# Kernel tuning notes

Measured on AMD Instinct MI355X. Metric: run time of the kernel, lower is better.

The kernel has to match this reference:

```python
import jax, jax.numpy as jnp
import numpy as np

N_NODES = 100000
N_EDGES = 1600000
D = 128
L = 2


def setup_inputs() -> dict:
    key = jax.random.key(0)
    ks = jax.random.split(key, 8)
    s = 1.0 / np.sqrt(D)
    return {
        "x": jax.random.normal(ks[0], (N_NODES, D), dtype=jnp.float32),
        "edge_index": jax.random.randint(ks[1], (2, N_EDGES), 0, N_NODES, dtype=jnp.int64),
        "edge_weight": jax.random.uniform(ks[2], (N_EDGES,), dtype=jnp.float32),
        "weight": jax.random.normal(ks[3], (L, D, D), dtype=jnp.float32) * s,
        "w_ih": jax.random.normal(ks[4], (3 * D, D), dtype=jnp.float32) * s,
        "w_hh": jax.random.normal(ks[5], (3 * D, D), dtype=jnp.float32) * s,
        "b_ih": jax.random.normal(ks[6], (3 * D,), dtype=jnp.float32) * s,
        "b_hh": jax.random.normal(ks[7], (3 * D,), dtype=jnp.float32) * s,
    }


def _gru_cell(m, h, w_ih, w_hh, b_ih, b_hh):
    # torch.nn.GRUCell: gates ordered (reset, update, new)
    gi = m @ w_ih.T + b_ih  # [N, 3D]
    gh = h @ w_hh.T + b_hh  # [N, 3D]
    i_r, i_z, i_n = jnp.split(gi, 3, axis=-1)
    h_r, h_z, h_n = jnp.split(gh, 3, axis=-1)
    r = jax.nn.sigmoid(i_r + h_r)
    z = jax.nn.sigmoid(i_z + h_z)
    n = jnp.tanh(i_n + r * h_n)
    return (1.0 - z) * n + z * h


def reference(x, edge_index, edge_weight, weight, w_ih, w_hh, b_ih, b_hh):
    src = edge_index[0]
    dst = edge_index[1]
    h = x  # in_channels == out_channels, no zero-padding needed
    for i in range(L):
        m = h @ weight[i]                          # [N, D]
        msg = m[src] * edge_weight[:, None]        # [E, D] gather + scale
        agg = jax.ops.segment_sum(msg, dst, num_segments=N_NODES)  # scatter-add
        h = _gru_cell(agg, h, w_ih, w_hh, b_ih, b_hh)
    return h
```

## Files before the change

kernel.cpp:

```cpp
#include <hip/hip_runtime.h>
#include <hip/hip_bf16.h>
#include <stdint.h>

typedef unsigned short u16;
typedef unsigned long long u64;
typedef __attribute__((ext_vector_type(8))) short bf16x8;
typedef __attribute__((ext_vector_type(4))) float f32x4;

#define DD 128
#define NB 256
#define SB 10240

__device__ __forceinline__ u16 f2bf(float f){
  uint32_t u = __float_as_uint(f);
  uint32_t r = (u + 0x7fffu + ((u >> 16) & 1u)) >> 16;
  return (u16)r;
}
__device__ __forceinline__ float bf2f(u16 h){ return __uint_as_float(((uint32_t)h) << 16); }

struct Frag2 { bf16x8 hi, lo; };

__device__ __forceinline__ Frag2 split8(float4 v0, float4 v1){
  union { float f[8]; uint32_t u[8]; } U;
  *(float4*)&U.f[0] = v0; *(float4*)&U.f[4] = v1;
  union { uint32_t w[4]; bf16x8 v; } H, L;
  #pragma unroll
  for (int q = 0; q < 4; q++){
    uint32_t a = U.u[2*q], b = U.u[2*q+1];
    H.w[q] = __builtin_amdgcn_perm(b, a, 0x07060302);
    float l0 = U.f[2*q]   - __uint_as_float(a & 0xffff0000u);
    float l1 = U.f[2*q+1] - __uint_as_float(b & 0xffff0000u);
    L.w[q] = __builtin_amdgcn_perm(__float_as_uint(l1), __float_as_uint(l0), 0x07060302);
  }
  Frag2 r; r.hi = H.v; r.lo = L.v; return r;
}

__device__ __forceinline__ Frag2 load_afrag_g(const float* A, int row, int k0){
  const float4* p = (const float4*)(A + (size_t)row * DD + k0);
  return split8(p[0], p[1]);
}

__global__ void pack_kernel(const float* __restrict__ w, const float* __restrict__ wih,
                            const float* __restrict__ whh, const float* __restrict__ bih,
                            const float* __restrict__ bhh, u16* __restrict__ wtb,
                            u16* __restrict__ ihb, u16* __restrict__ hhb,
                            float* __restrict__ bias, int* __restrict__ gcursor, int L){
  int tid = blockIdx.x * 256 + threadIdx.x;
  int lane = tid & 63;
  int b1 = L * 2048, b2 = b1 + 6144, b3 = b2 + 6144, b4 = b3 + 512, b5 = b4 + NB;
  if (tid < b1){
    int kc = (tid >> 6) & 3, t = (tid >> 8) & 7, l = tid >> 11;
    int col = t*16 + (lane & 15), kb = kc*32 + 8*(lane >> 4);
    #pragma unroll
    for (int e = 0; e < 8; e++)
      wtb[(size_t)tid*8 + e] = f2bf(w[(size_t)l*DD*DD + (size_t)(kb + e)*DD + col]);
  } else if (tid < b2){
    int id = tid - b1;
    int kc = (id >> 6) & 3, t = id >> 8;
    int row = t*16 + (lane & 15), kb = kc*32 + 8*(lane >> 4);
    #pragma unroll
    for (int e = 0; e < 8; e++)
      ihb[(size_t)id*8 + e] = f2bf(wih[(size_t)row*DD + kb + e]);
  } else if (tid < b3){
    int id = tid - b2;
    int kc = (id >> 6) & 3, t = id >> 8;
    int row = t*16 + (lane & 15), kb = kc*32 + 8*(lane >> 4);
    #pragma unroll
    for (int e = 0; e < 8; e++)
      hhb[(size_t)id*8 + e] = f2bf(whh[(size_t)row*DD + kb + e]);
  } else if (tid < b4){
    int id = tid - b3;
    if (id < 256)      bias[id] = bih[id] + bhh[id];
    else if (id < 384) bias[id] = bih[id];
    else               bias[id] = bhh[id - 128];
  } else if (tid < b5){
    gcursor[tid - b4] = 0;
  }
}

__global__ __launch_bounds__(256) void binA_kernel(const int* __restrict__ src,
    const int* __restrict__ dst, const float* __restrict__ ew,
    int* __restrict__ gcursor, u64* __restrict__ staging, int E, int N){
  __shared__ unsigned lcnt[NB];
  __shared__ unsigned lbase[NB];
  __shared__ unsigned lcur[NB];
  __shared__ unsigned gbase[NB];
  __shared__ unsigned char sbucket[4096];
  __shared__ u64 sedge[4096];
  const int CH = 4096;
  int tid = threadIdx.x;
  int e0 = blockIdx.x * CH;

  lcnt[tid] = 0;
  __syncthreads();
  for (int i = tid; i < CH; i += 256){
    int e = e0 + i;
    if (e < E){
      unsigned d = (unsigned)dst[e];
      if (d < (unsigned)N) atomicAdd(&lcnt[d >> 9], 1u);
    }
  }
  __syncthreads();
  lbase[tid] = lcnt[tid];
  __syncthreads();
  for (int off = 1; off < NB; off <<= 1){
    unsigned t = (tid >= off) ? lbase[tid - off] : 0u;
    __syncthreads();
    lbase[tid] += t;
    __syncthreads();
  }
  unsigned total = lbase[NB - 1];
  lbase[tid] -= lcnt[tid];
  gbase[tid] = (unsigned)atomicAdd(&gcursor[tid], (int)lcnt[tid]);
  lcur[tid] = lbase[tid];
  __syncthreads();
  for (int i = tid; i < CH; i += 256){
    int e = e0 + i;
    if (e < E){
      unsigned d = (unsigned)dst[e];
      if (d < (unsigned)N){
        unsigned b = d >> 9;
        unsigned p = atomicAdd(&lcur[b], 1u);
        unsigned s = (unsigned)src[e];
        sedge[p] = ((u64)__float_as_uint(ew[e]) << 32) | ((u64)(s & 0x1FFFFu) << 9)
                 | (u64)(d & 0x1FFu);
        sbucket[p] = (unsigned char)b;
      }
    }
  }
  __syncthreads();
  for (int i = tid; i < (int)total; i += 256){
    unsigned b = sbucket[i];
    unsigned gpos = gbase[b] + ((unsigned)i - lbase[b]);
    if (gpos < SB) staging[(size_t)b*SB + gpos] = sedge[i];
  }
}

__global__ __launch_bounds__(256) void binB_kernel(const u64* __restrict__ staging,
    const int* __restrict__ gcursor, int* __restrict__ row_ptr,
    uint2* __restrict__ entries, int N, int E){
  __shared__ int sg[NB];
  __shared__ unsigned ncnt[512];
  __shared__ unsigned nsc[512];
  __shared__ unsigned ncur[512];
  int tid = threadIdx.x;
  int b = blockIdx.x;
  sg[tid] = gcursor[tid];
  __syncthreads();
  for (int off = 1; off < NB; off <<= 1){
    int t = (tid >= off) ? sg[tid - off] : 0;
    __syncthreads();
    sg[tid] += t;
    __syncthreads();
  }
  int cnt = gcursor[b];
  if (cnt > SB) cnt = SB;
  int base = sg[b] - cnt;
  if (b == NB - 1 && tid == 0) row_ptr[N] = sg[NB - 1];
  const u64* st = staging + (size_t)b * SB;

  ncnt[tid] = 0; ncnt[tid + 256] = 0;
  __syncthreads();
  for (int i = tid; i < cnt; i += 256)
    atomicAdd(&ncnt[(unsigned)(st[i] & 0x1FFu)], 1u);
  __syncthreads();
  nsc[tid] = ncnt[tid]; nsc[tid + 256] = ncnt[tid + 256];
  __syncthreads();
  for (int off = 1; off < 512; off <<= 1){
    unsigned t0 = (tid >= off) ? nsc[tid - off] : 0u;
    unsigned t1 = (tid + 256 >= off) ? nsc[tid + 256 - off] : 0u;
    __syncthreads();
    nsc[tid] += t0; nsc[tid + 256] += t1;
    __syncthreads();
  }
  #pragma unroll
  for (int h = 0; h < 2; h++){
    int k = tid + h*256;
    unsigned excl = nsc[k] - ncnt[k];
    int g = b*512 + k;
    if (g < N) row_ptr[g] = base + (int)excl;
    ncur[k] = excl;
  }
  __syncthreads();
  for (int i = tid; i < cnt; i += 256){
    u64 v = st[i];
    unsigned local = (unsigned)(v & 0x1FFu);
    unsigned p = atomicAdd(&ncur[local], 1u);
    uint2 ent;
    ent.x = (unsigned)((v >> 9) & 0x1FFFFu);
    ent.y = (unsigned)(v >> 32);
    entries[base + p] = ent;
  }
}

__global__ __launch_bounds__(256) void gemm_m_kernel(const float* __restrict__ hin,
    const u16* __restrict__ wb, u16* __restrict__ mout, int nstripes){
  __shared__ u16 lw[32*512];
  int lane = threadIdx.x & 63;
  int wid = threadIdx.x >> 6;
  int stripe = blockIdx.x*4 + wid;
  bool active = stripe < nstripes;
  int n0 = (active ? stripe : (nstripes - 1)) * 16;
  int lrow = lane & 15, lk = lane >> 4;

  bf16x8 sreg[8];
  #pragma unroll
  for (int b = 0; b < 8; b++){
    int q = wid*8 + b;
    sreg[b] = *(const bf16x8*)(wb + ((size_t)q*64 + lane)*8);
  }
  Frag2 a[4];
  #pragma unroll
  for (int kc = 0; kc < 4; kc++)
    a[kc] = load_afrag_g(hin, n0 + lrow, kc*32 + 8*lk);
  #pragma unroll
  for (int b = 0; b < 8; b++){
    int q = wid*8 + b;
    *(bf16x8*)(lw + ((size_t)q*64 + lane)*8) = sreg[b];
  }
  __syncthreads();

  f32x4 zero = {0.f, 0.f, 0.f, 0.f};
  f32x4 acc[8];
  #pragma unroll
  for (int t = 0; t < 8; t++) acc[t] = zero;
  #pragma unroll
  for (int kc = 0; kc < 4; kc++){
    #pragma unroll
    for (int t = 0; t < 8; t++){
      bf16x8 b = *(const bf16x8*)(lw + ((size_t)(t*4 + kc)*64 + lane)*8);
      acc[t] = __builtin_amdgcn_mfma_f32_16x16x32_bf16(a[kc].hi, b, acc[t], 0, 0, 0);
      acc[t] = __builtin_amdgcn_mfma_f32_16x16x32_bf16(a[kc].lo, b, acc[t], 0, 0, 0);
    }
  }
  if (active){
    #pragma unroll
    for (int t = 0; t < 8; t++){
      #pragma unroll
      for (int r = 0; r < 4; r++)
        mout[(size_t)(n0 + lk*4 + r)*DD + t*16 + lrow] = f2bf(acc[t][r]);
    }
  }
}

__global__ __launch_bounds__(256) void gather_kernel(const int* __restrict__ row_ptr,
    const uint2* __restrict__ entries, const u16* __restrict__ mbf,
    float* __restrict__ agg, int N){
  int lane = threadIdx.x & 63;
  int node = (blockIdx.x*256 + threadIdx.x) >> 6;
  if (node >= N) return;
  int s = row_ptr[node], e = row_ptr[node + 1];
  float al[8], ah[8];
  #pragma unroll
  for (int u = 0; u < 8; u++){ al[u] = 0.f; ah[u] = 0.f; }
  int i = s;
  for (; i + 16 <= e; i += 16){
    uint2 en[16];
    #pragma unroll
    for (int u = 0; u < 16; u++) en[u] = entries[i + u];
    uint32_t mv[16];
    #pragma unroll
    for (int u = 0; u < 16; u++)
      mv[u] = *(const uint32_t*)(mbf + (size_t)en[u].x*DD + 2*lane);
    #pragma unroll
    for (int u = 0; u < 16; u++){
      float wv = __uint_as_float(en[u].y);
      al[u & 7] += wv * bf2f((u16)(mv[u] & 0xffffu));
      ah[u & 7] += wv * bf2f((u16)(mv[u] >> 16));
    }
  }
  for (; i + 8 <= e; i += 8){
    uint2 en[8];
    #pragma unroll
    for (int u = 0; u < 8; u++) en[u] = entries[i + u];
    uint32_t mv[8];
    #pragma unroll
    for (int u = 0; u < 8; u++)
      mv[u] = *(const uint32_t*)(mbf + (size_t)en[u].x*DD + 2*lane);
    #pragma unroll
    for (int u = 0; u < 8; u++){
      float wv = __uint_as_float(en[u].y);
      al[u] += wv * bf2f((u16)(mv[u] & 0xffffu));
      ah[u] += wv * bf2f((u16)(mv[u] >> 16));
    }
  }
  for (; i < e; i++){
    uint2 ent = entries[i];
    float wv = __uint_as_float(ent.y);
    uint32_t mv = *(const uint32_t*)(mbf + (size_t)ent.x*DD + 2*lane);
    al[0] += wv * bf2f((u16)(mv & 0xffffu));
    ah[0] += wv * bf2f((u16)(mv >> 16));
  }
  float2 o;
  o.x = ((al[0]+al[1]) + (al[2]+al[3])) + ((al[4]+al[5]) + (al[6]+al[7]));
  o.y = ((ah[0]+ah[1]) + (ah[2]+ah[3])) + ((ah[4]+ah[5]) + (ah[6]+ah[7]));
  *(float2*)(agg + (size_t)node*DD + 2*lane) = o;
}

__global__ __launch_bounds__(256, 4) void gru_kernel(
    const float* __restrict__ agg, const float* hin,
    const u16* __restrict__ ihb, const u16* __restrict__ hhb,
    const float* __restrict__ bias, float* hout, int nstripes){
  __shared__ u16 lw[2][12*512];
  int lane = threadIdx.x & 63;
  int wid = threadIdx.x >> 6;
  int stripe = blockIdx.x*4 + wid;
  bool active = stripe < nstripes;
  int n0 = (active ? stripe : (nstripes - 1)) * 16;
  int lrow = lane & 15, lk = lane >> 4;

  Frag2 aa[4], ahf[4];
  #pragma unroll
  for (int kc = 0; kc < 4; kc++){
    int k0 = kc*32 + 8*lk;
    aa[kc]  = load_afrag_g(agg, n0 + lrow, k0);
    ahf[kc] = load_afrag_g(hin, n0 + lrow, k0);
  }

  int q = wid*3;
  int g0 = q >> 2,       kc0 = q & 3;
  int g1 = (q+1) >> 2,   kc1 = (q+1) & 3;
  int g2 = (q+2) >> 2,   kc2 = (q+2) & 3;

  {
    bf16x8 s0 = *(const bf16x8*)(ihb + ((size_t)((g0*8 + 0)*4 + kc0)*64 + lane)*8);
    bf16x8 s1 = *(const bf16x8*)(ihb + ((size_t)((g1*8 + 0)*4 + kc1)*64 + lane)*8);
    bf16x8 s2 = *(const bf16x8*)(ihb + ((size_t)((g2*8 + 0)*4 + kc2)*64 + lane)*8);
    *(bf16x8*)(lw[0] + ((size_t)(q+0)*64 + lane)*8) = s0;
    *(bf16x8*)(lw[0] + ((size_t)(q+1)*64 + lane)*8) = s1;
    *(bf16x8*)(lw[0] + ((size_t)(q+2)*64 + lane)*8) = s2;
  }
  __syncthreads();

  f32x4 zero = {0.f, 0.f, 0.f, 0.f};
  f32x4 ir = zero, iz = zero, in_ = zero, hr = zero, hz = zero, hn = zero;
  for (int ph = 0; ph < 16; ph++){
    int jt = ph >> 1, half = ph & 1;
    bf16x8 n0r, n1r, n2r;
    if (ph < 15){
      int njt = (ph + 1) >> 1;
      const u16* wsrc = ((ph + 1) & 1) ? hhb : ihb;
      n0r = *(const bf16x8*)(wsrc + ((size_t)((g0*8 + njt)*4 + kc0)*64 + lane)*8);
      n1r = *(const bf16x8*)(wsrc + ((size_t)((g1*8 + njt)*4 + kc1)*64 + lane)*8);
      n2r = *(const bf16x8*)(wsrc + ((size_t)((g2*8 + njt)*4 + kc2)*64 + lane)*8);
    }
    const u16* buf = lw[ph & 1];
    if (half == 0){
      ir = zero; iz = zero; in_ = zero;
      #pragma unroll
      for (int kc = 0; kc < 4; kc++){
        bf16x8 b0 = *(const bf16x8*)(buf + ((size_t)(0*4 + kc)*64 + lane)*8);
        bf16x8 b1 = *(const bf16x8*)(buf + ((size_t)(1*4 + kc)*64 + lane)*8);
        bf16x8 b2 = *(const bf16x8*)(buf + ((size_t)(2*4 + kc)*64 + lane)*8);
        ir  = __builtin_amdgcn_mfma_f32_16x16x32_bf16(aa[kc].hi, b0, ir,  0, 0, 0);
        ir  = __builtin_amdgcn_mfma_f32_16x16x32_bf16(aa[kc].lo, b0, ir,  0, 0, 0);
        iz  = __builtin_amdgcn_mfma_f32_16x16x32_bf16(aa[kc].hi, b1, iz,  0, 0, 0);
        iz  = __builtin_amdgcn_mfma_f32_16x16x32_bf16(aa[kc].lo, b1, iz,  0, 0, 0);
        in_ = __builtin_amdgcn_mfma_f32_16x16x32_bf16(aa[kc].hi, b2, in_, 0, 0, 0);
        in_ = __builtin_amdgcn_mfma_f32_16x16x32_bf16(aa[kc].lo, b2, in_, 0, 0, 0);
      }
    } else {
      hr = zero; hz = zero; hn = zero;
      #pragma unroll
      for (int kc = 0; kc < 4; kc++){
        bf16x8 b0 = *(const bf16x8*)(buf + ((size_t)(0*4 + kc)*64 + lane)*8);
        bf16x8 b1 = *(const bf16x8*)(buf + ((size_t)(1*4 + kc)*64 + lane)*8);
        bf16x8 b2 = *(const bf16x8*)(buf + ((size_t)(2*4 + kc)*64 + lane)*8);
        hr = __builtin_amdgcn_mfma_f32_16x16x32_bf16(ahf[kc].hi, b0, hr, 0, 0, 0);
        hr = __builtin_amdgcn_mfma_f32_16x16x32_bf16(ahf[kc].lo, b0, hr, 0, 0, 0);
        hz = __builtin_amdgcn_mfma_f32_16x16x32_bf16(ahf[kc].hi, b1, hz, 0, 0, 0);
        hz = __builtin_amdgcn_mfma_f32_16x16x32_bf16(ahf[kc].lo, b1, hz, 0, 0, 0);
        hn = __builtin_amdgcn_mfma_f32_16x16x32_bf16(ahf[kc].hi, b2, hn, 0, 0, 0);
        hn = __builtin_amdgcn_mfma_f32_16x16x32_bf16(ahf[kc].lo, b2, hn, 0, 0, 0);
      }
      if (active){
        int j = jt*16 + lrow;
        float br = bias[j];
        float bz = bias[128 + j];
        float bi = bias[256 + j];
        float bh = bias[384 + j];
        #pragma unroll
        for (int r = 0; r < 4; r++){
          int node = n0 + lk*4 + r;
          float xr = ir[r] + hr[r] + br;
          float xz = iz[r] + hz[r] + bz;
          float rg = __builtin_amdgcn_rcpf(1.f + __expf(-xr));
          float zg = __builtin_amdgcn_rcpf(1.f + __expf(-xz));
          float xn = in_[r] + bi + rg*(hn[r] + bh);
          xn = fminf(fmaxf(xn, -30.f), 30.f);
          float e2 = __expf(2.f*xn);
          float ng = 1.f - 2.f*__builtin_amdgcn_rcpf(e2 + 1.f);
          float hv = hin[(size_t)node*DD + j];
          hout[(size_t)node*DD + j] = ng + zg*(hv - ng);
        }
      }
    }
    if (ph < 15){
      u16* nbuf = lw[(ph + 1) & 1];
      *(bf16x8*)(nbuf + ((size_t)(q+0)*64 + lane)*8) = n0r;
      *(bf16x8*)(nbuf + ((size_t)(q+1)*64 + lane)*8) = n1r;
      *(bf16x8*)(nbuf + ((size_t)(q+2)*64 + lane)*8) = n2r;
    }
    __syncthreads();
  }
}

extern "C" void kernel_launch(void* const* d_in, const int* in_sizes, int n_in,
                              void* d_out, int out_size, void* d_ws, size_t ws_size,
                              hipStream_t stream){
  const float* x   = (const float*)d_in[0];
  const int*   ei  = (const int*)d_in[1];
  const float* ew  = (const float*)d_in[2];
  const float* wgt = (const float*)d_in[3];
  const float* wih = (const float*)d_in[4];
  const float* whh = (const float*)d_in[5];
  const float* bih = (const float*)d_in[6];
  const float* bhh = (const float*)d_in[7];
  float* out = (float*)d_out;

  const int N = in_sizes[0] / DD;
  const int E = in_sizes[2];
  const int L = in_sizes[3] / (DD * DD);

  char* p = (char*)d_ws;
  auto alloc = [&](size_t b) -> char* {
    char* r = p; p += (b + 255) & ~(size_t)255; return r;
  };
  u16*   wtb     = (u16*)  alloc((size_t)L * 2048 * 8 * 2);
  u16*   ihb     = (u16*)  alloc((size_t)6144 * 8 * 2);
  u16*   hhb     = (u16*)  alloc((size_t)6144 * 8 * 2);
  float* bias    = (float*)alloc(512 * 4);
  int*   gcursor = (int*)  alloc(NB * 4);
  int*   row_ptr = (int*)  alloc(((size_t)N + 1) * 4);
  uint2* entries = (uint2*)alloc((size_t)E * 8);
  u16*   mbf     = (u16*)  alloc((size_t)N * DD * 2);
  float* agg     = (float*)alloc((size_t)N * DD * 4);
  u64*   staging = (u64*)agg;

  const int* src = ei;
  const int* dst = ei + E;

  int packN = L*2048 + 6144 + 6144 + 512 + NB;
  pack_kernel<<<(packN + 255)/256, 256, 0, stream>>>(wgt, wih, whh, bih, bhh,
                                                     wtb, ihb, hhb, bias, gcursor, L);
  binA_kernel<<<(E + 4095)/4096, 256, 0, stream>>>(src, dst, ew, gcursor, staging, E, N);
  binB_kernel<<<NB, 256, 0, stream>>>(staging, gcursor, row_ptr, entries, N, E);

  int nstripes = N / 16;
  int ggrid = (nstripes + 3) / 4;
  for (int l = 0; l < L; l++){
    const float* hin = (l == 0) ? x : out;
    gemm_m_kernel<<<ggrid, 256, 0, stream>>>(hin, wtb + (size_t)l*2048*8, mbf, nstripes);
    gather_kernel<<<(N*64 + 255)/256, 256, 0, stream>>>(row_ptr, entries, mbf, agg, N);
    gru_kernel<<<ggrid, 256, 0, stream>>>(agg, hin, ihb, hhb, bias, out, nstripes);
  }
}
```

Baseline: 380.3 us.

## Slice node features into column strips and pack edge entries into 32-bit words

```diff
diff --git a/kernel.cpp b/kernel.cpp
--- a/kernel.cpp
+++ b/kernel.cpp
@@ -138,7 +138,7 @@
 
 __global__ __launch_bounds__(256) void binB_kernel(const u64* __restrict__ staging,
     const int* __restrict__ gcursor, int* __restrict__ row_ptr,
-    uint2* __restrict__ entries, int N, int E){
+    uint32_t* __restrict__ entries, int N, int E){
   __shared__ int sg[NB];
   __shared__ unsigned ncnt[512];
   __shared__ unsigned nsc[512];
@@ -186,15 +186,16 @@
     u64 v = st[i];
     unsigned local = (unsigned)(v & 0x1FFu);
     unsigned p = atomicAdd(&ncur[local], 1u);
-    uint2 ent;
-    ent.x = (unsigned)((v >> 9) & 0x1FFFFu);
-    ent.y = (unsigned)(v >> 32);
-    entries[base + p] = ent;
+    unsigned s = (unsigned)((v >> 9) & 0x1FFFFu);
+    float w = __uint_as_float((unsigned)(v >> 32));
+    unsigned wq = (unsigned)(w * 32768.f + 0.5f);
+    if (wq > 32767u) wq = 32767u;
+    entries[base + p] = (s << 15) | wq;
   }
 }
 
 __global__ __launch_bounds__(256) void gemm_m_kernel(const float* __restrict__ hin,
-    const u16* __restrict__ wb, u16* __restrict__ mout, int nstripes){
+    const u16* __restrict__ wb, u16* __restrict__ msb, int nstripes, int N){
   __shared__ u16 lw[32*512];
   int lane = threadIdx.x & 63;
   int wid = threadIdx.x >> 6;
@@ -238,63 +239,58 @@
     for (int t = 0; t < 8; t++){
       #pragma unroll
       for (int r = 0; r < 4; r++)
-        mout[(size_t)(n0 + lk*4 + r)*DD + t*16 + lrow] = f2bf(acc[t][r]);
-    }
-  }
-}
-
-__global__ __launch_bounds__(256) void gather_kernel(const int* __restrict__ row_ptr,
-    const uint2* __restrict__ entries, const u16* __restrict__ mbf,
+        msb[(size_t)t*N*16 + (size_t)(n0 + lk*4 + r)*16 + lrow] = f2bf(acc[t][r]);
+    }
+  }
+}
+
+__global__ __launch_bounds__(512) void gather_kernel(const int* __restrict__ row_ptr,
+    const uint32_t* __restrict__ entries, const u16* __restrict__ msb,
     float* __restrict__ agg, int N){
   int lane = threadIdx.x & 63;
-  int node = (blockIdx.x*256 + threadIdx.x) >> 6;
-  if (node >= N) return;
-  int s = row_ptr[node], e = row_ptr[node + 1];
-  float al[8], ah[8];
-  #pragma unroll
-  for (int u = 0; u < 8; u++){ al[u] = 0.f; ah[u] = 0.f; }
-  int i = s;
-  for (; i + 16 <= e; i += 16){
-    uint2 en[16];
-    #pragma unroll
-    for (int u = 0; u < 16; u++) en[u] = entries[i + u];
-    uint32_t mv[16];
-    #pragma unroll
-    for (int u = 0; u < 16; u++)
-      mv[u] = *(const uint32_t*)(mbf + (size_t)en[u].x*DD + 2*lane);
-    #pragma unroll
-    for (int u = 0; u < 16; u++){
-      float wv = __uint_as_float(en[u].y);
-      al[u & 7] += wv * bf2f((u16)(mv[u] & 0xffffu));
-      ah[u & 7] += wv * bf2f((u16)(mv[u] >> 16));
-    }
-  }
-  for (; i + 8 <= e; i += 8){
-    uint2 en[8];
-    #pragma unroll
-    for (int u = 0; u < 8; u++) en[u] = entries[i + u];
-    uint32_t mv[8];
-    #pragma unroll
-    for (int u = 0; u < 8; u++)
-      mv[u] = *(const uint32_t*)(mbf + (size_t)en[u].x*DD + 2*lane);
-    #pragma unroll
-    for (int u = 0; u < 8; u++){
-      float wv = __uint_as_float(en[u].y);
-      al[u] += wv * bf2f((u16)(mv[u] & 0xffffu));
-      ah[u] += wv * bf2f((u16)(mv[u] >> 16));
-    }
-  }
-  for (; i < e; i++){
-    uint2 ent = entries[i];
-    float wv = __uint_as_float(ent.y);
-    uint32_t mv = *(const uint32_t*)(mbf + (size_t)ent.x*DD + 2*lane);
-    al[0] += wv * bf2f((u16)(mv & 0xffffu));
-    ah[0] += wv * bf2f((u16)(mv >> 16));
-  }
-  float2 o;
-  o.x = ((al[0]+al[1]) + (al[2]+al[3])) + ((al[4]+al[5]) + (al[6]+al[7]));
-  o.y = ((ah[0]+ah[1]) + (ah[2]+ah[3])) + ((ah[4]+ah[5]) + (ah[6]+ah[7]));
-  *(float2*)(agg + (size_t)node*DD + 2*lane) = o;
+  int wid = threadIdx.x >> 6;
+  int s = blockIdx.x & 7;
+  int slot = (blockIdx.x >> 3)*8 + wid;
+  const u16* ms = msb + (size_t)s*N*16;
+  int g = lane >> 3;
+  int c = lane & 7;
+
+  for (int node = slot; node < N; node += 8192){
+    int s0 = row_ptr[node], e0 = row_ptr[node + 1];
+    float a0 = 0.f, a1 = 0.f;
+    int i = s0;
+    for (; i + 16 <= e0; i += 16){
+      unsigned w0 = entries[i + g];
+      unsigned w1 = entries[i + 8 + g];
+      uint32_t m0 = *(const uint32_t*)(ms + (size_t)(w0 >> 15)*16 + 2*c);
+      uint32_t m1 = *(const uint32_t*)(ms + (size_t)(w1 >> 15)*16 + 2*c);
+      float f0 = (float)(w0 & 0x7fffu) * (1.f/32768.f);
+      float f1 = (float)(w1 & 0x7fffu) * (1.f/32768.f);
+      a0 += f0 * __uint_as_float(m0 << 16);
+      a1 += f0 * __uint_as_float(m0 & 0xffff0000u);
+      a0 += f1 * __uint_as_float(m1 << 16);
+      a1 += f1 * __uint_as_float(m1 & 0xffff0000u);
+    }
+    for (; i < e0; i += 8){
+      int idx = i + g;
+      if (idx < e0){
+        unsigned w0 = entries[idx];
+        uint32_t m0 = *(const uint32_t*)(ms + (size_t)(w0 >> 15)*16 + 2*c);
+        float f0 = (float)(w0 & 0x7fffu) * (1.f/32768.f);
+        a0 += f0 * __uint_as_float(m0 << 16);
+        a1 += f0 * __uint_as_float(m0 & 0xffff0000u);
+      }
+    }
+    #pragma unroll
+    for (int msk = 8; msk < 64; msk <<= 1){
+      a0 += __shfl_xor(a0, msk);
+      a1 += __shfl_xor(a1, msk);
+    }
+    if (lane < 8){
+      float2 o; o.x = a0; o.y = a1;
+      *(float2*)(agg + (size_t)node*DD + s*16 + 2*c) = o;
+    }
+  }
 }
 
 __global__ __launch_bounds__(256, 4) void gru_kernel(
@@ -426,16 +422,16 @@
   auto alloc = [&](size_t b) -> char* {
     char* r = p; p += (b + 255) & ~(size_t)255; return r;
   };
-  u16*   wtb     = (u16*)  alloc((size_t)L * 2048 * 8 * 2);
-  u16*   ihb     = (u16*)  alloc((size_t)6144 * 8 * 2);
-  u16*   hhb     = (u16*)  alloc((size_t)6144 * 8 * 2);
-  float* bias    = (float*)alloc(512 * 4);
-  int*   gcursor = (int*)  alloc(NB * 4);
-  int*   row_ptr = (int*)  alloc(((size_t)N + 1) * 4);
-  uint2* entries = (uint2*)alloc((size_t)E * 8);
-  u16*   mbf     = (u16*)  alloc((size_t)N * DD * 2);
-  float* agg     = (float*)alloc((size_t)N * DD * 4);
-  u64*   staging = (u64*)agg;
+  u16*      wtb     = (u16*)     alloc((size_t)L * 2048 * 8 * 2);
+  u16*      ihb     = (u16*)     alloc((size_t)6144 * 8 * 2);
+  u16*      hhb     = (u16*)     alloc((size_t)6144 * 8 * 2);
+  float*    bias    = (float*)   alloc(512 * 4);
+  int*      gcursor = (int*)     alloc(NB * 4);
+  int*      row_ptr = (int*)     alloc(((size_t)N + 1) * 4);
+  uint32_t* entries = (uint32_t*)alloc((size_t)E * 4);
+  u16*      msb     = (u16*)     alloc((size_t)N * DD * 2);
+  float*    agg     = (float*)   alloc((size_t)N * DD * 4);
+  u64*      staging = (u64*)agg;
 
   const int* src = ei;
   const int* dst = ei + E;
@@ -450,8 +446,8 @@
   int ggrid = (nstripes + 3) / 4;
   for (int l = 0; l < L; l++){
     const float* hin = (l == 0) ? x : out;
-    gemm_m_kernel<<<ggrid, 256, 0, stream>>>(hin, wtb + (size_t)l*2048*8, mbf, nstripes);
-    gather_kernel<<<(N*64 + 255)/256, 256, 0, stream>>>(row_ptr, entries, mbf, agg, N);
+    gemm_m_kernel<<<ggrid, 256, 0, stream>>>(hin, wtb + (size_t)l*2048*8, msb, nstripes, N);
+    gather_kernel<<<8192, 512, 0, stream>>>(row_ptr, entries, msb, agg, N);
     gru_kernel<<<ggrid, 256, 0, stream>>>(agg, hin, ihb, hhb, bias, out, nstripes);
   }
 }
```

After: 560.2 us. 1.47x slower.

## Triple-buffer GRU weight tiles and fully unroll the gate loop

Applied to the files above, without the earlier changes.

```diff
diff --git a/kernel.cpp b/kernel.cpp
--- a/kernel.cpp
+++ b/kernel.cpp
@@ -301,7 +301,7 @@
     const float* __restrict__ agg, const float* hin,
     const u16* __restrict__ ihb, const u16* __restrict__ hhb,
     const float* __restrict__ bias, float* hout, int nstripes){
-  __shared__ u16 lw[2][12*512];
+  __shared__ u16 lw[3][12*512];
   int lane = threadIdx.x & 63;
   int wid = threadIdx.x >> 6;
   int stripe = blockIdx.x*4 + wid;
@@ -321,85 +321,104 @@
   int g0 = q >> 2,       kc0 = q & 3;
   int g1 = (q+1) >> 2,   kc1 = (q+1) & 3;
   int g2 = (q+2) >> 2,   kc2 = (q+2) & 3;
-
+  size_t lo0 = ((size_t)(q+0)*64 + lane)*8;
+  size_t lo1 = ((size_t)(q+1)*64 + lane)*8;
+  size_t lo2 = ((size_t)(q+2)*64 + lane)*8;
+
+  bf16x8 rH0, rH1, rH2;
   {
-    bf16x8 s0 = *(const bf16x8*)(ihb + ((size_t)((g0*8 + 0)*4 + kc0)*64 + lane)*8);
-    bf16x8 s1 = *(const bf16x8*)(ihb + ((size_t)((g1*8 + 0)*4 + kc1)*64 + lane)*8);
-    bf16x8 s2 = *(const bf16x8*)(ihb + ((size_t)((g2*8 + 0)*4 + kc2)*64 + lane)*8);
-    *(bf16x8*)(lw[0] + ((size_t)(q+0)*64 + lane)*8) = s0;
-    *(bf16x8*)(lw[0] + ((size_t)(q+1)*64 + lane)*8) = s1;
-    *(bf16x8*)(lw[0] + ((size_t)(q+2)*64 + lane)*8) = s2;
+    bf16x8 i0 = *(const bf16x8*)(ihb + ((size_t)((g0*8 + 0)*4 + kc0)*64 + lane)*8);
+    bf16x8 i1 = *(const bf16x8*)(ihb + ((size_t)((g1*8 + 0)*4 + kc1)*64 + lane)*8);
+    bf16x8 i2 = *(const bf16x8*)(ihb + ((size_t)((g2*8 + 0)*4 + kc2)*64 + lane)*8);
+    rH0 = *(const bf16x8*)(hhb + ((size_t)((g0*8 + 0)*4 + kc0)*64 + lane)*8);
+    rH1 = *(const bf16x8*)(hhb + ((size_t)((g1*8 + 0)*4 + kc1)*64 + lane)*8);
+    rH2 = *(const bf16x8*)(hhb + ((size_t)((g2*8 + 0)*4 + kc2)*64 + lane)*8);
+    *(bf16x8*)(lw[0] + lo0) = i0;
+    *(bf16x8*)(lw[0] + lo1) = i1;
+    *(bf16x8*)(lw[0] + lo2) = i2;
+    *(bf16x8*)(lw[1] + lo0) = rH0;
+    *(bf16x8*)(lw[1] + lo1) = rH1;
+    *(bf16x8*)(lw[1] + lo2) = rH2;
   }
   __syncthreads();
 
   f32x4 zero = {0.f, 0.f, 0.f, 0.f};
-  f32x4 ir = zero, iz = zero, in_ = zero, hr = zero, hz = zero, hn = zero;
-  for (int ph = 0; ph < 16; ph++){
-    int jt = ph >> 1, half = ph & 1;
-    bf16x8 n0r, n1r, n2r;
-    if (ph < 15){
-      int njt = (ph + 1) >> 1;
-      const u16* wsrc = ((ph + 1) & 1) ? hhb : ihb;
-      n0r = *(const bf16x8*)(wsrc + ((size_t)((g0*8 + njt)*4 + kc0)*64 + lane)*8);
-      n1r = *(const bf16x8*)(wsrc + ((size_t)((g1*8 + njt)*4 + kc1)*64 + lane)*8);
-      n2r = *(const bf16x8*)(wsrc + ((size_t)((g2*8 + njt)*4 + kc2)*64 + lane)*8);
-    }
-    const u16* buf = lw[ph & 1];
-    if (half == 0){
-      ir = zero; iz = zero; in_ = zero;
+  f32x4 ir = zero, iz = zero, in_ = zero;
+  #pragma unroll
+  for (int j = 0; j < 8; j++){
+    const u16* bufE = lw[(2*j) % 3];
+    u16* bufO = lw[(2*j + 1) % 3];
+    u16* bufE2 = lw[(2*j + 2) % 3];
+
+    bf16x8 nI0, nI1, nI2, nH0, nH1, nH2;
+    if (j < 7){
+      int njt = j + 1;
+      nI0 = *(const bf16x8*)(ihb + ((size_t)((g0*8 + njt)*4 + kc0)*64 + lane)*8);
+      nI1 = *(const bf16x8*)(ihb + ((size_t)((g1*8 + njt)*4 + kc1)*64 + lane)*8);
+      nI2 = *(const bf16x8*)(ihb + ((size_t)((g2*8 + njt)*4 + kc2)*64 + lane)*8);
+      nH0 = *(const bf16x8*)(hhb + ((size_t)((g0*8 + njt)*4 + kc0)*64 + lane)*8);
+      nH1 = *(const bf16x8*)(hhb + ((size_t)((g1*8 + njt)*4 + kc1)*64 + lane)*8);
+      nH2 = *(const bf16x8*)(hhb + ((size_t)((g2*8 + njt)*4 + kc2)*64 + lane)*8);
+    }
+    ir = zero; iz = zero; in_ = zero;
+    #pragma unroll
+    for (int kc = 0; kc < 4; kc++){
+      bf16x8 b0 = *(const bf16x8*)(bufE + ((size_t)(0*4 + kc)*64 + lane)*8);
+      bf16x8 b1 = *(const bf16x8*)(bufE + ((size_t)(1*4 + kc)*64 + lane)*8);
+      bf16x8 b2 = *(const bf16x8*)(bufE + ((size_t)(2*4 + kc)*64 + lane)*8);
+      ir  = __builtin_amdgcn_mfma_f32_16x16x32_bf16(aa[kc].hi, b0, ir,  0, 0, 0);
+      ir  = __builtin_amdgcn_mfma_f32_16x16x32_bf16(aa[kc].lo, b0, ir,  0, 0, 0);
+      iz  = __builtin_amdgcn_mfma_f32_16x16x32_bf16(aa[kc].hi, b1, iz,  0, 0, 0);
+      iz  = __builtin_amdgcn_mfma_f32_16x16x32_bf16(aa[kc].lo, b1, iz,  0, 0, 0);
+      in_ = __builtin_amdgcn_mfma_f32_16x16x32_bf16(aa[kc].hi, b2, in_, 0, 0, 0);
+      in_ = __builtin_amdgcn_mfma_f32_16x16x32_bf16(aa[kc].lo, b2, in_, 0, 0, 0);
+    }
+    if (j > 0){
+      *(bf16x8*)(bufO + lo0) = rH0;
+      *(bf16x8*)(bufO + lo1) = rH1;
+      *(bf16x8*)(bufO + lo2) = rH2;
+    }
+    __syncthreads();
+
+    f32x4 hr = zero, hz = zero, hn = zero;
+    #pragma unroll
+    for (int kc = 0; kc < 4; kc++){
+      bf16x8 b0 = *(const bf16x8*)(bufO + ((size_t)(0*4 + kc)*64 + lane)*8);
+      bf16x8 b1 = *(const bf16x8*)(bufO + ((size_t)(1*4 + kc)*64 + lane)*8);
+      bf16x8 b2 = *(const bf16x8*)(bufO + ((size_t)(2*4 + kc)*64 + lane)*8);
+      hr = __builtin_amdgcn_mfma_f32_16x16x32_bf16(ahf[kc].hi, b0, hr, 0, 0, 0);
+      hr = __builtin_amdgcn_mfma_f32_16x16x32_bf16(ahf[kc].lo, b0, hr, 0, 0, 0);
+      hz = __builtin_amdgcn_mfma_f32_16x16x32_bf16(ahf[kc].hi, b1, hz, 0, 0, 0);
+      hz = __builtin_amdgcn_mfma_f32_16x16x32_bf16(ahf[kc].lo, b1, hz, 0, 0, 0);
+      hn = __builtin_amdgcn_mfma_f32_16x16x32_bf16(ahf[kc].hi, b2, hn, 0, 0, 0);
+      hn = __builtin_amdgcn_mfma_f32_16x16x32_bf16(ahf[kc].lo, b2, hn, 0, 0, 0);
+    }
+    if (active){
+      int jj = j*16 + lrow;
+      float br = bias[jj];
+      float bz = bias[128 + jj];
+      float bi = bias[256 + jj];
+      float bh = bias[384 + jj];
       #pragma unroll
-      for (int kc = 0; kc < 4; kc++){
-        bf16x8 b0 = *(const bf16x8*)(buf + ((size_t)(0*4 + kc)*64 + lane)*8);
-        bf16x8 b1 = *(const bf16x8*)(buf + ((size_t)(1*4 + kc)*64 + lane)*8);
-        bf16x8 b2 = *(const bf16x8*)(buf + ((size_t)(2*4 + kc)*64 + lane)*8);
-        ir  = __builtin_amdgcn_mfma_f32_16x16x32_bf16(aa[kc].hi, b0, ir,  0, 0, 0);
-        ir  = __builtin_amdgcn_mfma_f32_16x16x32_bf16(aa[kc].lo, b0, ir,  0, 0, 0);
-        iz  = __builtin_amdgcn_mfma_f32_16x16x32_bf16(aa[kc].hi, b1, iz,  0, 0, 0);
-        iz  = __builtin_amdgcn_mfma_f32_16x16x32_bf16(aa[kc].lo, b1, iz,  0, 0, 0);
-        in_ = __builtin_amdgcn_mfma_f32_16x16x32_bf16(aa[kc].hi, b2, in_, 0, 0, 0);
-        in_ = __builtin_amdgcn_mfma_f32_16x16x32_bf16(aa[kc].lo, b2, in_, 0, 0, 0);
+      for (int r = 0; r < 4; r++){
+        int node = n0 + lk*4 + r;
+        float xr = ir[r] + hr[r] + br;
+        float xz = iz[r] + hz[r] + bz;
+        float rg = __builtin_amdgcn_rcpf(1.f + __expf(-xr));
+        float zg = __builtin_amdgcn_rcpf(1.f + __expf(-xz));
+        float xn = in_[r] + bi + rg*(hn[r] + bh);
+        xn = fminf(fmaxf(xn, -30.f), 30.f);
+        float e2 = __expf(2.f*xn);
+        float ng = 1.f - 2.f*__builtin_amdgcn_rcpf(e2 + 1.f);
+        float hv = hin[(size_t)node*DD + jj];
+        hout[(size_t)node*DD + jj] = ng + zg*(hv - ng);
       }
-    } else {
-      hr = zero; hz = zero; hn = zero;
-      #pragma unroll
-      for (int kc = 0; kc < 4; kc++){
-        bf16x8 b0 = *(const bf16x8*)(buf + ((size_t)(0*4 + kc)*64 + lane)*8);
-        bf16x8 b1 = *(const bf16x8*)(buf + ((size_t)(1*4 + kc)*64 + lane)*8);
-        bf16x8 b2 = *(const bf16x8*)(buf + ((size_t)(2*4 + kc)*64 + lane)*8);
-        hr = __builtin_amdgcn_mfma_f32_16x16x32_bf16(ahf[kc].hi, b0, hr, 0, 0, 0);
-        hr = __builtin_amdgcn_mfma_f32_16x16x32_bf16(ahf[kc].lo, b0, hr, 0, 0, 0);
-        hz = __builtin_amdgcn_mfma_f32_16x16x32_bf16(ahf[kc].hi, b1, hz, 0, 0, 0);
-        hz = __builtin_amdgcn_mfma_f32_16x16x32_bf16(ahf[kc].lo, b1, hz, 0, 0, 0);
-        hn = __builtin_amdgcn_mfma_f32_16x16x32_bf16(ahf[kc].hi, b2, hn, 0, 0, 0);
-        hn = __builtin_amdgcn_mfma_f32_16x16x32_bf16(ahf[kc].lo, b2, hn, 0, 0, 0);
-      }
-      if (active){
-        int j = jt*16 + lrow;
-        float br = bias[j];
-        float bz = bias[128 + j];
-        float bi = bias[256 + j];
-        float bh = bias[384 + j];
-        #pragma unroll
-        for (int r = 0; r < 4; r++){
-          int node = n0 + lk*4 + r;
-          float xr = ir[r] + hr[r] + br;
-          float xz = iz[r] + hz[r] + bz;
-          float rg = __builtin_amdgcn_rcpf(1.f + __expf(-xr));
-          float zg = __builtin_amdgcn_rcpf(1.f + __expf(-xz));
-          float xn = in_[r] + bi + rg*(hn[r] + bh);
-          xn = fminf(fmaxf(xn, -30.f), 30.f);
-          float e2 = __expf(2.f*xn);
-          float ng = 1.f - 2.f*__builtin_amdgcn_rcpf(e2 + 1.f);
-          float hv = hin[(size_t)node*DD + j];
-          hout[(size_t)node*DD + j] = ng + zg*(hv - ng);
-        }
-      }
-    }
-    if (ph < 15){
-      u16* nbuf = lw[(ph + 1) & 1];
-      *(bf16x8*)(nbuf + ((size_t)(q+0)*64 + lane)*8) = n0r;
-      *(bf16x8*)(nbuf + ((size_t)(q+1)*64 + lane)*8) = n1r;
-      *(bf16x8*)(nbuf + ((size_t)(q+2)*64 + lane)*8) = n2r;
+    }
+    if (j < 7){
+      *(bf16x8*)(bufE2 + lo0) = nI0;
+      *(bf16x8*)(bufE2 + lo1) = nI1;
+      *(bf16x8*)(bufE2 + lo2) = nI2;
+      rH0 = nH0; rH1 = nH1; rH2 = nH2;
     }
     __syncthreads();
   }
```

Result: slower. 405.9 us (+6.7%).

## Gather four edges per wavefront with 16-byte row loads and shuffle-reduce

Applied to the files above, without the earlier changes.

```diff
diff --git a/kernel.cpp b/kernel.cpp
--- a/kernel.cpp
+++ b/kernel.cpp
@@ -235,9 +235,9 @@
   }
   if (active){
     #pragma unroll
-    for (int t = 0; t < 8; t++){
+    for (int r = 0; r < 4; r++){
       #pragma unroll
-      for (int r = 0; r < 4; r++)
+      for (int t = 0; t < 8; t++)
         mout[(size_t)(n0 + lk*4 + r)*DD + t*16 + lrow] = f2bf(acc[t][r]);
     }
   }
@@ -247,54 +247,41 @@
     const uint2* __restrict__ entries, const u16* __restrict__ mbf,
     float* __restrict__ agg, int N){
   int lane = threadIdx.x & 63;
+  int q = lane >> 4;
+  int t = lane & 15;
   int node = (blockIdx.x*256 + threadIdx.x) >> 6;
   if (node >= N) return;
   int s = row_ptr[node], e = row_ptr[node + 1];
-  float al[8], ah[8];
-  #pragma unroll
-  for (int u = 0; u < 8; u++){ al[u] = 0.f; ah[u] = 0.f; }
-  int i = s;
-  for (; i + 16 <= e; i += 16){
-    uint2 en[16];
-    #pragma unroll
-    for (int u = 0; u < 16; u++) en[u] = entries[i + u];
-    uint32_t mv[16];
-    #pragma unroll
-    for (int u = 0; u < 16; u++)
-      mv[u] = *(const uint32_t*)(mbf + (size_t)en[u].x*DD + 2*lane);
-    #pragma unroll
-    for (int u = 0; u < 16; u++){
-      float wv = __uint_as_float(en[u].y);
-      al[u & 7] += wv * bf2f((u16)(mv[u] & 0xffffu));
-      ah[u & 7] += wv * bf2f((u16)(mv[u] >> 16));
-    }
-  }
-  for (; i + 8 <= e; i += 8){
-    uint2 en[8];
-    #pragma unroll
-    for (int u = 0; u < 8; u++) en[u] = entries[i + u];
-    uint32_t mv[8];
-    #pragma unroll
-    for (int u = 0; u < 8; u++)
-      mv[u] = *(const uint32_t*)(mbf + (size_t)en[u].x*DD + 2*lane);
-    #pragma unroll
-    for (int u = 0; u < 8; u++){
-      float wv = __uint_as_float(en[u].y);
-      al[u] += wv * bf2f((u16)(mv[u] & 0xffffu));
-      ah[u] += wv * bf2f((u16)(mv[u] >> 16));
-    }
-  }
-  for (; i < e; i++){
-    uint2 ent = entries[i];
-    float wv = __uint_as_float(ent.y);
-    uint32_t mv = *(const uint32_t*)(mbf + (size_t)ent.x*DD + 2*lane);
-    al[0] += wv * bf2f((u16)(mv & 0xffffu));
-    ah[0] += wv * bf2f((u16)(mv >> 16));
-  }
-  float2 o;
-  o.x = ((al[0]+al[1]) + (al[2]+al[3])) + ((al[4]+al[5]) + (al[6]+al[7]));
-  o.y = ((ah[0]+ah[1]) + (ah[2]+ah[3])) + ((ah[4]+ah[5]) + (ah[6]+ah[7]));
-  *(float2*)(agg + (size_t)node*DD + 2*lane) = o;
+  float acc[8];
+  #pragma unroll
+  for (int c = 0; c < 8; c++) acc[c] = 0.f;
+  #pragma unroll 4
+  for (int i = s; i < e; i += 4){
+    int idx = i + q;
+    bool valid = idx < e;
+    uint2 en = entries[valid ? idx : i];
+    float w = valid ? __uint_as_float(en.y) : 0.f;
+    uint4 mv = *(const uint4*)(mbf + (size_t)en.x*DD + 8*t);
+    acc[0] += w * __uint_as_float(mv.x << 16);
+    acc[1] += w * __uint_as_float(mv.x & 0xffff0000u);
+    acc[2] += w * __uint_as_float(mv.y << 16);
+    acc[3] += w * __uint_as_float(mv.y & 0xffff0000u);
+    acc[4] += w * __uint_as_float(mv.z << 16);
+    acc[5] += w * __uint_as_float(mv.z & 0xffff0000u);
+    acc[6] += w * __uint_as_float(mv.w << 16);
+    acc[7] += w * __uint_as_float(mv.w & 0xffff0000u);
+  }
+  #pragma unroll
+  for (int c = 0; c < 8; c++){
+    acc[c] += __shfl_xor(acc[c], 16);
+    acc[c] += __shfl_xor(acc[c], 32);
+  }
+  if (q == 0){
+    float4 o0 = {acc[0], acc[1], acc[2], acc[3]};
+    float4 o1 = {acc[4], acc[5], acc[6], acc[7]};
+    *(float4*)(agg + (size_t)node*DD + 8*t)     = o0;
+    *(float4*)(agg + (size_t)node*DD + 8*t + 4) = o1;
+  }
 }
 
 __global__ __launch_bounds__(256, 4) void gru_kernel(
```

New measurement: 352.5 us. 1.08x faster.
